# Optimization experiments

Measured on AMD Instinct MI355X. Metric: run time of the kernel, lower is better.

Reference implementation:

```python
import jax, jax.numpy as jnp
import numpy as np

SPIRAL_LEN = 12
V_LEVELS = [32768, 8192, 2048, 512, 128]
CHANNELS = [3, 32, 64, 128, 256]


def spiral_conv(x, spiral, W, b):
    # x: [B, V, C_in]; spiral: [V, S] neighbor indices
    B, V, C = x.shape
    g = x[:, spiral, :]                      # [B, V, S, C_in] irregular gather
    g = g.reshape(B, V, -1)                  # [B, V, S*C_in]
    return g @ W + b                         # [B, V, C_out]


def mesh_pool(x, idx, w):
    # sparse down_transform (<=3 nnz per row): out[b,i,:] = sum_k w[i,k] * x[b, idx[i,k], :]
    return jnp.einsum('bvkc,vk->bvc', x[:, idx, :], w)


def setup_inputs() -> dict:
    key = jax.random.key(0)
    ks = jax.random.split(key, 32)
    S = SPIRAL_LEN
    V = V_LEVELS
    C = CHANNELS
    d = {}
    d['x'] = jax.random.normal(ks[0], (32, V[0], C[0]), dtype=jnp.float32)
    for i in range(4):
        d[f'spiral{i}'] = jax.random.randint(ks[1 + i], (V[i], S), 0, V[i])
        d[f'didx{i}'] = jax.random.randint(ks[5 + i], (V[i + 1], 3), 0, V[i])
        w = jax.random.uniform(ks[9 + i], (V[i + 1], 3), dtype=jnp.float32)
        d[f'dw{i}'] = w / w.sum(-1, keepdims=True)  # barycentric-like rows
        fan_in = S * C[i]
        d[f'W{i}'] = jax.random.normal(ks[13 + i], (fan_in, C[i + 1]), dtype=jnp.float32) * np.float32(1.0 / np.sqrt(fan_in))
        d[f'b{i}'] = jnp.zeros((C[i + 1],), jnp.float32)
    flat_in = V[4] * C[4]  # num_vert * out_channels[-2]
    d['Wl1'] = jax.random.normal(ks[20], (flat_in, 512), dtype=jnp.float32) * np.float32(1.0 / np.sqrt(flat_in))
    d['bl1'] = jnp.zeros((512,), jnp.float32)
    d['Wl2'] = jax.random.normal(ks[21], (512, 64), dtype=jnp.float32) * np.float32(1.0 / np.sqrt(512))
    d['bl2'] = jnp.zeros((64,), jnp.float32)
    return d


def reference(x, spiral0, spiral1, spiral2, spiral3,
              didx0, didx1, didx2, didx3,
              dw0, dw1, dw2, dw3,
              W0, b0, W1, b1, W2, b2, W3, b3,
              Wl1, bl1, Wl2, bl2):
    spirals = (spiral0, spiral1, spiral2, spiral3)
    didx = (didx0, didx1, didx2, didx3)
    dw = (dw0, dw1, dw2, dw3)
    Wb = ((W0, b0), (W1, b1), (W2, b2), (W3, b3))
    for i in range(4):  # SpiralEnblock: elu(spiral_conv(x)) -> sparse pool
        x = jax.nn.elu(spiral_conv(x, spirals[i], *Wb[i]))
        x = mesh_pool(x, didx[i], dw[i])
    B = x.shape[0]
    x = x.reshape(B, -1)                     # [B, num_vert * C_last]
    x = jax.nn.elu(x @ Wl1 + bl1)            # [B, 512]
    y = x @ Wl2 + bl2                        # [B, latent]
    return (x, y)
```

## Files before the change

kernel.cpp:

```cpp
#include <hip/hip_runtime.h>
#include <cstdint>
#include <cstddef>

typedef _Float16 f16x8 __attribute__((ext_vector_type(8)));
typedef _Float16 f16x4 __attribute__((ext_vector_type(4)));
typedef float f32x4 __attribute__((ext_vector_type(4)));

static __device__ __forceinline__ float elu_f(float t) {
    return t > 0.0f ? t : expm1f(t);
}

static __device__ __forceinline__ int block_pu0(int bid, int P, int vshift_out, int nbl)
{
    if (nbl < 0) return bid * P;
    int xcd  = bid & 7;
    int slot = bid >> 3;
    int nb   = slot & ((1 << nbl) - 1);
    int tile = slot >> nbl;
    return ((xcd + (nb << 3)) << vshift_out) + tile * P;
}

template<int KTOT, int C_OUT, int BN>
__global__ __launch_bounds__(256)
void prep_w(const float* __restrict__ W, _Float16* __restrict__ o)
{
    constexpr int KT = KTOT/64;
    int i = blockIdx.x * 256 + threadIdx.x;
    if (i >= KTOT*C_OUT) return;
    int j = i & 7;
    int rest = i >> 3;
    int n = rest % BN;
    int kc = (rest / BN) & 7;
    int t = (rest / (BN*8)) % KT;
    int y = rest / (BN*8*KT);
    int k = t*64 + kc*8 + j;
    o[i] = (_Float16)W[(size_t)k*C_OUT + y*BN + n];
}

__global__ __launch_bounds__(256)
void prep_w0(const float* __restrict__ W, _Float16* __restrict__ o)
{
    int i = blockIdx.x * 256 + threadIdx.x;
    if (i >= 2048) return;
    int j = i & 7;
    int n = (i >> 3) & 31;
    int kc = i >> 8;
    int k = kc*8 + j;
    int s = k >> 2, c = k & 3;
    float v = (s < 12 && c < 3) ? W[(size_t)(s*3 + c)*32 + n] : 0.0f;
    o[i] = (_Float16)v;
}

__global__ __launch_bounds__(256)
void prep_xT(const float* __restrict__ x, _Float16* __restrict__ xT)
{
    __shared__ _Float16 t[16][64*4 + 8];
    const int v0 = blockIdx.x * 64;
    const int tid = threadIdx.x;
    #pragma unroll
    for (int it = 0; it < 4; ++it) {
        int e = it*256 + tid;
        int b = e >> 6, v = e & 63;
        const float* p = x + ((size_t)b*32768 + v0 + v)*3;
        f16x4 h;
        h[0] = (_Float16)p[0]; h[1] = (_Float16)p[1];
        h[2] = (_Float16)p[2]; h[3] = (_Float16)0.f;
        *(f16x4*)&t[b][v*4] = h;
    }
    __syncthreads();
    #pragma unroll
    for (int it = 0; it < 2; ++it) {
        int e = it*256 + tid;
        int vl = e >> 3, s = e & 7;
        f16x4 a = *(const f16x4*)&t[2*s][vl*4];
        f16x4 b = *(const f16x4*)&t[2*s+1][vl*4];
        f16x8 h;
        h[0]=a[0]; h[1]=a[1]; h[2]=a[2]; h[3]=a[3];
        h[4]=b[0]; h[5]=b[1]; h[6]=b[2]; h[7]=b[3];
        *(f16x8*)&xT[((size_t)(v0+vl)*16 + s*2)*4] = h;
    }
}

__global__ __launch_bounds__(256)
void prep_gidx(const int* __restrict__ didx, const int* __restrict__ spiral,
               unsigned int* __restrict__ g)
{
    int i = blockIdx.x*256 + threadIdx.x;
    if (i >= 24576*8) return;
    int q = i & 7;
    int row = i >> 3;
    unsigned int val = 0;
    if (q < 6) {
        int v = didx[row];
        unsigned int s0 = (unsigned int)spiral[v*12 + q*2];
        unsigned int s1 = (unsigned int)spiral[v*12 + q*2 + 1];
        val = s0 | (s1 << 16);
    }
    g[i] = val;
}

__global__ __launch_bounds__(256)
void conv0T(const _Float16* __restrict__ xT, const unsigned int* __restrict__ gidx,
            const _Float16* __restrict__ Wp, const float* __restrict__ bias,
            const float* __restrict__ dwt, _Float16* __restrict__ out)
{
    __shared__ _Float16 Ep[4][512];
    const int tid  = threadIdx.x;
    const int wave = tid >> 6;
    const int lane = tid & 63;
    const int quad = lane >> 4;
    const int l16  = lane & 15;
    const int u0   = blockIdx.x * 8 + wave * 2;

    f16x8 bf[2][2];
    #pragma unroll
    for (int kt = 0; kt < 2; ++kt)
        #pragma unroll
        for (int nt = 0; nt < 2; ++nt)
            bf[kt][nt] = *(const f16x8*)&Wp[(((kt*4+quad)*32) + nt*16 + l16)*8];
    float bv[2] = { bias[l16], bias[16 + l16] };

    #pragma unroll
    for (int ui = 0; ui < 2; ++ui) {
        int u = u0 + ui;
        f32x4 pacc[2] = {{0.f,0.f,0.f,0.f},{0.f,0.f,0.f,0.f}};
        #pragma unroll
        for (int kp = 0; kp < 3; ++kp) {
            int r = u*3 + kp;
            unsigned int gp0 = gidx[r*8 + quad];
            unsigned int gp1 = gidx[r*8 + 4 + quad];
            f16x4 a0 = *(const f16x4*)&xT[(size_t)(gp0 & 0xffffu)*64 + l16*4];
            f16x4 a1 = *(const f16x4*)&xT[(size_t)(gp0 >> 16)*64 + l16*4];
            f16x4 a2 = *(const f16x4*)&xT[(size_t)(gp1 & 0xffffu)*64 + l16*4];
            f16x4 a3 = *(const f16x4*)&xT[(size_t)(gp1 >> 16)*64 + l16*4];
            f16x8 af0, af1;
            af0[0]=a0[0]; af0[1]=a0[1]; af0[2]=a0[2]; af0[3]=a0[3];
            af0[4]=a1[0]; af0[5]=a1[1]; af0[6]=a1[2]; af0[7]=a1[3];
            af1[0]=a2[0]; af1[1]=a2[1]; af1[2]=a2[2]; af1[3]=a2[3];
            af1[4]=a3[0]; af1[5]=a3[1]; af1[6]=a3[2]; af1[7]=a3[3];
            float dw = dwt[r];
            #pragma unroll
            for (int nt = 0; nt < 2; ++nt) {
                f32x4 m = {0.f,0.f,0.f,0.f};
                m = __builtin_amdgcn_mfma_f32_16x16x32_f16(af0, bf[0][nt], m, 0,0,0);
                m = __builtin_amdgcn_mfma_f32_16x16x32_f16(af1, bf[1][nt], m, 0,0,0);
                #pragma unroll
                for (int rr = 0; rr < 4; ++rr)
                    pacc[nt][rr] += dw * elu_f(m[rr] + bv[nt]);
            }
        }
        #pragma unroll
        for (int nt = 0; nt < 2; ++nt)
            #pragma unroll
            for (int rr = 0; rr < 4; ++rr)
                Ep[wave][(quad*4+rr)*32 + nt*16 + l16] = (_Float16)pacc[nt][rr];
        int b  = lane >> 2;
        int c8 = lane & 3;
        f16x8 rowv = *(const f16x8*)&Ep[wave][b*32 + c8*8];
        *(f16x8*)&out[(size_t)b*262144 + (size_t)u*32 + c8*8] = rowv;
    }
}

template<int C_IN, int C_OUT, int P, int BN, int WGM, int WGN, bool OUT_HALF>
__global__ __launch_bounds__(256)
void conv_pool_mfma(const _Float16* __restrict__ x, const int* __restrict__ spiral,
                    const _Float16* __restrict__ Wp, const float* __restrict__ bias,
                    const int* __restrict__ didx, const float* __restrict__ dwt,
                    void* __restrict__ outv, int vshift_in, int vshift_out, int nbl)
{
    constexpr int R    = 3*P;
    constexpr int KTOT = 12*C_IN;
    constexpr int KT   = KTOT/64;
    constexpr int NST  = KT*2;
    constexpr int WTM  = R/WGM;
    constexpr int WTN  = BN/WGN;
    constexpr int NMT  = WTM/16;
    constexpr int NNT  = WTN/16;
    constexpr int C4   = BN/4;
    static_assert(WTM % 16 == 0 && WTN % 16 == 0, "tile");
    static_assert(R <= 256 && (P*C4) % 256 == 0, "loops");

    __shared__ unsigned short gidx[R*12];
    __shared__ _Float16 E[R*(BN+4)];

    const int tid  = threadIdx.x;
    const int wave = tid >> 6;
    const int lane = tid & 63;
    const int quad = lane >> 4;
    const int l16  = lane & 15;
    const int wm   = wave / WGN;
    const int wn   = wave % WGN;
    const int pu0  = block_pu0(blockIdx.x, P, vshift_out, nbl);
    const int n0   = blockIdx.y * BN;
    const int vmask_out = (1 << vshift_out) - 1;
    const int base_in = (pu0 >> vshift_out) << vshift_in;

    if (tid < R) {
        int ul = tid / 3;
        int kp = tid - ul*3;
        int u  = (pu0 + ul) & vmask_out;
        int v  = didx[u*3 + kp];
        const int* svp = spiral + v*12;
        #pragma unroll
        for (int j = 0; j < 12; ++j) gidx[tid*12 + j] = (unsigned short)svp[j];
    }
    __syncthreads();

    f32x4 acc[NMT][NNT];
    #pragma unroll
    for (int i = 0; i < NMT; ++i)
        #pragma unroll
        for (int j = 0; j < NNT; ++j) acc[i][j] = (f32x4){0.f, 0.f, 0.f, 0.f};

    const _Float16* xb = x + (size_t)base_in * C_IN;

    auto loadStep = [&](int s, f16x8* af, f16x8* bf) {
        const int k0 = s*32;
        const int sv = k0 / C_IN;
        const int c  = (k0 & (C_IN-1)) + quad*8;
        #pragma unroll
        for (int i = 0; i < NMT; ++i) {
            int m_local = wm*WTM + i*16 + l16;
            int g = gidx[m_local*12 + sv];
            af[i] = *(const f16x8*)&xb[(size_t)g*C_IN + c];
        }
        const _Float16* wsrc = Wp + ((size_t)(blockIdx.y*NST + s)*4 + quad)*BN*8;
        #pragma unroll
        for (int j = 0; j < NNT; ++j) {
            int n_local = wn*WTN + j*16 + l16;
            bf[j] = *(const f16x8*)&wsrc[n_local*8];
        }
    };
    auto mfmaStep = [&](const f16x8* af, const f16x8* bf) {
        #pragma unroll
        for (int i = 0; i < NMT; ++i)
            #pragma unroll
            for (int j = 0; j < NNT; ++j)
                acc[i][j] = __builtin_amdgcn_mfma_f32_16x16x32_f16(
                    af[i], bf[j], acc[i][j], 0, 0, 0);
    };

    f16x8 afA[NMT], bfA[NNT], afB[NMT], bfB[NNT];
    loadStep(0, afA, bfA);
    for (int st = 0; st < NST; st += 2) {
        loadStep(st + 1, afB, bfB);
        mfmaStep(afA, bfA);
        if (st + 2 < NST) loadStep(st + 2, afA, bfA);
        mfmaStep(afB, bfB);
    }

    float bv[NNT];
    #pragma unroll
    for (int j = 0; j < NNT; ++j)
        bv[j] = bias[n0 + wn*WTN + j*16 + l16];

    #pragma unroll
    for (int i = 0; i < NMT; ++i) {
        int row_base = wm*WTM + i*16 + quad*4;
        #pragma unroll
        for (int j = 0; j < NNT; ++j) {
            int col = wn*WTN + j*16 + l16;
            #pragma unroll
            for (int r = 0; r < 4; ++r)
                E[(size_t)(row_base + r)*(BN+4) + col] =
                    (_Float16)elu_f(acc[i][j][r] + bv[j]);
        }
    }
    __syncthreads();

    #pragma unroll
    for (int e = tid; e < P*C4; e += 256) {
        int ul = e / C4;
        int c4 = e - ul*C4;
        int pu = pu0 + ul;
        int u  = pu & vmask_out;
        const float* w = dwt + u*3;
        f16x4 a0 = *(const f16x4*)&E[(size_t)(ul*3 + 0)*(BN+4) + c4*4];
        f16x4 a1 = *(const f16x4*)&E[(size_t)(ul*3 + 1)*(BN+4) + c4*4];
        f16x4 a2 = *(const f16x4*)&E[(size_t)(ul*3 + 2)*(BN+4) + c4*4];
        float ox = w[0]*(float)a0[0] + w[1]*(float)a1[0] + w[2]*(float)a2[0];
        float oy = w[0]*(float)a0[1] + w[1]*(float)a1[1] + w[2]*(float)a2[1];
        float oz = w[0]*(float)a0[2] + w[1]*(float)a1[2] + w[2]*(float)a2[2];
        float ow = w[0]*(float)a0[3] + w[1]*(float)a1[3] + w[2]*(float)a2[3];
        if (OUT_HALF) {
            f16x4 h; h[0]=(_Float16)ox; h[1]=(_Float16)oy; h[2]=(_Float16)oz; h[3]=(_Float16)ow;
            *(f16x4*)&((_Float16*)outv)[(size_t)pu*C_OUT + n0 + c4*4] = h;
        } else {
            float4 o; o.x=ox; o.y=oy; o.z=oz; o.w=ow;
            *(float4*)&((float*)outv)[(size_t)pu*C_OUT + n0 + c4*4] = o;
        }
    }
}

__global__ __launch_bounds__(256)
void fc1_partial(const float* __restrict__ xflat, const float* __restrict__ Wl1,
                 float* __restrict__ partial)
{
    __shared__ float sb[8704];
    const int tid = threadIdx.x;
    const int n4 = tid & 31;
    const int kq = (tid >> 5) & 3;
    const int mh = tid >> 7;
    const int nt = blockIdx.x;
    const int ks = blockIdx.y;
    const int kbase = ks * 128;

    for (int e = tid; e < 1024; e += 256) {
        int m = e >> 5, k4 = e & 31;
        *(float4*)&sb[m*128 + k4*4] = *(const float4*)&xflat[(size_t)m*32768 + kbase + k4*4];
    }
    __syncthreads();

    float acc[16][4];
    #pragma unroll
    for (int m = 0; m < 16; ++m)
        #pragma unroll
        for (int c = 0; c < 4; ++c) acc[m][c] = 0.0f;

    const float* Wb = Wl1 + (size_t)(kbase + kq*32)*512 + nt*128 + n4*4;
    #pragma unroll 2
    for (int i = 0; i < 32; i += 4) {
        float4 w0 = *(const float4*)(Wb + (size_t)(i+0)*512);
        float4 w1 = *(const float4*)(Wb + (size_t)(i+1)*512);
        float4 w2 = *(const float4*)(Wb + (size_t)(i+2)*512);
        float4 w3 = *(const float4*)(Wb + (size_t)(i+3)*512);
        #pragma unroll
        for (int m = 0; m < 16; ++m) {
            float4 xv = *(const float4*)&sb[(mh*16 + m)*128 + kq*32 + i];
            acc[m][0] += xv.x*w0.x + xv.y*w1.x + xv.z*w2.x + xv.w*w3.x;
            acc[m][1] += xv.x*w0.y + xv.y*w1.y + xv.z*w2.y + xv.w*w3.y;
            acc[m][2] += xv.x*w0.z + xv.y*w1.z + xv.z*w2.z + xv.w*w3.z;
            acc[m][3] += xv.x*w0.w + xv.y*w1.w + xv.z*w2.w + xv.w*w3.w;
        }
    }
    __syncthreads();

    int slot = (mh*2 + (kq >> 1))*32 + n4;
    if (kq & 1) {
        #pragma unroll
        for (int m = 0; m < 16; ++m)
            *(float4*)&sb[slot*68 + m*4] = *(float4*)&acc[m][0];
    }
    __syncthreads();
    if (!(kq & 1)) {
        #pragma unroll
        for (int m = 0; m < 16; ++m) {
            float4 v = *(const float4*)&sb[slot*68 + m*4];
            acc[m][0] += v.x; acc[m][1] += v.y; acc[m][2] += v.z; acc[m][3] += v.w;
        }
    }
    __syncthreads();
    int slot2 = mh*32 + n4;
    if (kq == 2) {
        #pragma unroll
        for (int m = 0; m < 16; ++m)
            *(float4*)&sb[slot2*68 + m*4] = *(float4*)&acc[m][0];
    }
    __syncthreads();
    if (kq == 0) {
        float* pb = partial + ((size_t)(ks*4 + nt)*32 + mh*16)*128 + n4*4;
        #pragma unroll
        for (int m = 0; m < 16; ++m) {
            float4 v = *(const float4*)&sb[slot2*68 + m*4];
            float4 o;
            o.x = acc[m][0] + v.x; o.y = acc[m][1] + v.y;
            o.z = acc[m][2] + v.z; o.w = acc[m][3] + v.w;
            *(float4*)(pb + (size_t)m*128) = o;
        }
    }
}

__global__ __launch_bounds__(256)
void fc1_reduce(const float* __restrict__ partial, const float* __restrict__ bl1,
                float* __restrict__ hout)
{
    int i = blockIdx.x * 256 + threadIdx.x;
    int m = i >> 9, n = i & 511;
    int nt = n >> 7, nl = n & 127;
    const float* p = partial + ((size_t)nt*32 + m)*128 + nl;
    float s = 0.0f;
    #pragma unroll 8
    for (int ks = 0; ks < 256; ++ks)
        s += p[(size_t)ks*4*4096];
    hout[i] = elu_f(s + bl1[n]);
}

__global__ __launch_bounds__(64)
void fc2_kernel(const float* __restrict__ h, const float* __restrict__ Wl2,
                const float* __restrict__ bl2, float* __restrict__ y)
{
    int m = blockIdx.x;
    int n = threadIdx.x;
    float s = bl2[n];
    for (int k = 0; k < 512; ++k)
        s += h[(size_t)m*512 + k] * Wl2[(size_t)k*64 + n];
    y[(size_t)m*64 + n] = s;
}

extern "C" void kernel_launch(void* const* d_in, const int* in_sizes, int n_in,
                              void* d_out, int out_size, void* d_ws, size_t ws_size,
                              hipStream_t stream)
{
    (void)in_sizes; (void)n_in; (void)out_size; (void)ws_size;

    const float* x0 = (const float*)d_in[0];
    const int*   sp[4]; const int* didx[4]; const float* dwp[4];
    const float* Wp[4]; const float* bp[4];
    for (int i = 0; i < 4; ++i) {
        sp[i]   = (const int*)  d_in[1 + i*5 + 0];
        didx[i] = (const int*)  d_in[1 + i*5 + 1];
        dwp[i]  = (const float*)d_in[1 + i*5 + 2];
        Wp[i]   = (const float*)d_in[1 + i*5 + 3];
        bp[i]   = (const float*)d_in[1 + i*5 + 4];
    }
    const float* Wl1 = (const float*)d_in[21];
    const float* bl1 = (const float*)d_in[22];
    const float* Wl2 = (const float*)d_in[23];
    const float* bl2 = (const float*)d_in[24];
    float* out = (float*)d_out;

    char* wsb = (char*)d_ws;
    float* persist      = (float*)wsb;
    float* partial      = (float*)(wsb + (4<<20));
    _Float16* xT        = (_Float16*)(wsb + (24<<20));
    _Float16* pooled0   = (_Float16*)(wsb + (32<<20));
    _Float16* pooled1   = (_Float16*)(wsb + (48<<20));
    _Float16* pooled2   = (_Float16*)(wsb + (56<<20));
    unsigned int* gidx0 = (unsigned int*)(wsb + (60<<20));
    _Float16* w0h       = (_Float16*)(wsb + (61<<20));
    _Float16* w1h       = w0h + 2048;
    _Float16* w2h       = w1h + 24576;
    _Float16* w3h       = w2h + 98304;

    prep_w0<<<8, 256, 0, stream>>>(Wp[0], w0h);
    prep_w< 384,  64,  64><<<( 24576 + 255)/256, 256, 0, stream>>>(Wp[1], w1h);
    prep_w< 768, 128, 128><<<( 98304 + 255)/256, 256, 0, stream>>>(Wp[2], w2h);
    prep_w<1536, 256,  64><<<(393216 + 255)/256, 256, 0, stream>>>(Wp[3], w3h);
    prep_gidx<<<768, 256, 0, stream>>>(didx[0], sp[0], gidx0);

    for (int h = 0; h < 2; ++h) {
        _Float16* xTh = xT + (size_t)h*2097152;
        prep_xT<<<512, 256, 0, stream>>>(x0 + (size_t)h*16*98304, xTh);
        conv0T<<<1024, 256, 0, stream>>>(xTh, gidx0, w0h, bp[0], dwp[0],
                                         pooled0 + (size_t)h*16*262144);
    }

    conv_pool_mfma<32,64,64,64,4,1,true><<<1024, 256, 0, stream>>>(
        pooled0, sp[1], w1h, bp[1], didx[1], dwp[1], pooled1, 13, 11, 2);

    conv_pool_mfma<64,128,32,128,2,2,true><<<512, 256, 0, stream>>>(
        pooled1, sp[2], w2h, bp[2], didx[2], dwp[2], pooled2, 11, 9, 2);

    conv_pool_mfma<128,256,32,64,2,2,false><<<dim3(128, 4), 256, 0, stream>>>(
        pooled2, sp[3], w3h, bp[3], didx[3], dwp[3], persist, 9, 7, 2);

    fc1_partial<<<dim3(4, 256), 256, 0, stream>>>(persist, Wl1, partial);
    fc1_reduce<<<64, 256, 0, stream>>>(partial, bl1, out);

    fc2_kernel<<<32, 64, 0, stream>>>(out, Wl2, bl2, out + 16384);
}
```

Baseline: 332.1 us.

## Deepen conv_pool register prefetch to four stages and halve block tile sizes

Adds a templated four-deep register prefetch pipeline to the MFMA spiral-conv kernel, so three K-steps of gathered A and W fragments are in flight while one is being multiplied. It also halves the pooled-vertex tile per block, reshapes the wave grid, doubles the grid size of the three conv layers, and adds a min-4-blocks occupancy hint to launch bounds. The aim is to hide gather latency and raise occupancy. In exchange it uses more registers per thread, which the occupancy hint may force into spills, and smaller tiles give less reuse of weight fragments.

```diff
diff --git a/kernel.cpp b/kernel.cpp
--- a/kernel.cpp
+++ b/kernel.cpp
@@ -161,8 +161,8 @@
     }
 }
 
-template<int C_IN, int C_OUT, int P, int BN, int WGM, int WGN, bool OUT_HALF>
-__global__ __launch_bounds__(256)
+template<int C_IN, int C_OUT, int P, int BN, int WGM, int WGN, bool OUT_HALF, int PIPE>
+__global__ __launch_bounds__(256, 4)
 void conv_pool_mfma(const _Float16* __restrict__ x, const int* __restrict__ spiral,
                     const _Float16* __restrict__ Wp, const float* __restrict__ bias,
                     const int* __restrict__ didx, const float* __restrict__ dwt,
@@ -179,6 +179,9 @@
     constexpr int C4   = BN/4;
     static_assert(WTM % 16 == 0 && WTN % 16 == 0, "tile");
     static_assert(R <= 256 && (P*C4) % 256 == 0, "loops");
+    static_assert(PIPE == 2 || PIPE == 4, "pipe");
+    static_assert(PIPE != 2 || NST % 2 == 0, "pipe2");
+    static_assert(PIPE != 4 || NST % 4 == 0, "pipe4");
 
     __shared__ unsigned short gidx[R*12];
     __shared__ _Float16 E[R*(BN+4)];
@@ -240,13 +243,31 @@
                     af[i], bf[j], acc[i][j], 0, 0, 0);
     };
 
-    f16x8 afA[NMT], bfA[NNT], afB[NMT], bfB[NNT];
-    loadStep(0, afA, bfA);
-    for (int st = 0; st < NST; st += 2) {
-        loadStep(st + 1, afB, bfB);
-        mfmaStep(afA, bfA);
-        if (st + 2 < NST) loadStep(st + 2, afA, bfA);
-        mfmaStep(afB, bfB);
+    if constexpr (PIPE == 2) {
+        f16x8 afA[NMT], bfA[NNT], afB[NMT], bfB[NNT];
+        loadStep(0, afA, bfA);
+        for (int st = 0; st < NST; st += 2) {
+            loadStep(st + 1, afB, bfB);
+            mfmaStep(afA, bfA);
+            if (st + 2 < NST) loadStep(st + 2, afA, bfA);
+            mfmaStep(afB, bfB);
+        }
+    } else {
+        f16x8 afA[NMT], bfA[NNT], afB[NMT], bfB[NNT];
+        f16x8 afC[NMT], bfC[NNT], afD[NMT], bfD[NNT];
+        loadStep(0, afA, bfA);
+        loadStep(1, afB, bfB);
+        loadStep(2, afC, bfC);
+        for (int st = 0; st < NST; st += 4) {
+            loadStep(st + 3, afD, bfD);
+            mfmaStep(afA, bfA);
+            if (st + 4 < NST) loadStep(st + 4, afA, bfA);
+            mfmaStep(afB, bfB);
+            if (st + 5 < NST) loadStep(st + 5, afB, bfB);
+            mfmaStep(afC, bfC);
+            if (st + 6 < NST) loadStep(st + 6, afC, bfC);
+            mfmaStep(afD, bfD);
+        }
     }
 
     float bv[NNT];
@@ -445,13 +466,13 @@
                                          pooled0 + (size_t)h*16*262144);
     }
 
-    conv_pool_mfma<32,64,64,64,4,1,true><<<1024, 256, 0, stream>>>(
+    conv_pool_mfma<32,64,32,64,2,2,true,4><<<2048, 256, 0, stream>>>(
         pooled0, sp[1], w1h, bp[1], didx[1], dwp[1], pooled1, 13, 11, 2);
 
-    conv_pool_mfma<64,128,32,128,2,2,true><<<512, 256, 0, stream>>>(
+    conv_pool_mfma<64,128,16,128,1,4,true,4><<<1024, 256, 0, stream>>>(
         pooled1, sp[2], w2h, bp[2], didx[2], dwp[2], pooled2, 11, 9, 2);
 
-    conv_pool_mfma<128,256,32,64,2,2,false><<<dim3(128, 4), 256, 0, stream>>>(
+    conv_pool_mfma<128,256,16,64,1,4,false,4><<<dim3(256, 4), 256, 0, stream>>>(
         pooled2, sp[3], w3h, bp[3], didx[3], dwp[3], persist, 9, 7, 2);
 
     fc1_partial<<<dim3(4, 256), 256, 0, stream>>>(persist, Wl1, partial);
```

New measurement: 384.5 us. +15.8%, slower.

## Stage spiral-gathered A and weight tiles through LDS with async global_load_lds double buffering

Applied to the files above, without the earlier changes.

Replaces the register-level direct global loads of gathered activations and packed weights with asynchronous global_load_lds copies into double-buffered, XOR-swizzled LDS tiles. Each k-group is staged one iteration ahead while MFMAs consume the current buffer, and the epilogue buffer E now aliases the staging memory. The goal is to overlap the irregular gather latency with compute and cut per-lane global traffic. In exchange it adds a block barrier per group and raises LDS usage, which may reduce occupancy.

```diff
diff --git a/kernel.cpp b/kernel.cpp
--- a/kernel.cpp
+++ b/kernel.cpp
@@ -8,6 +8,13 @@
 
 static __device__ __forceinline__ float elu_f(float t) {
     return t > 0.0f ? t : expm1f(t);
+}
+
+typedef __attribute__((address_space(1))) const unsigned int guint;
+typedef __attribute__((address_space(3))) unsigned int       luint;
+static __device__ __forceinline__ void gload_lds16(const void* g, void* l)
+{
+    __builtin_amdgcn_global_load_lds((guint*)g, (luint*)l, 16, 0, 0);
 }
 
 static __device__ __forceinline__ int block_pu0(int bid, int P, int vshift_out, int nbl)
@@ -177,11 +184,29 @@
     constexpr int NMT  = WTM/16;
     constexpr int NNT  = WTN/16;
     constexpr int C4   = BN/4;
+    constexpr int GS   = (C_IN == 32) ? 1 : 2;
+    constexpr int NG   = NST / GS;
+    constexpr int CPR  = GS * 4;
+    constexpr int CPRS = (CPR == 4) ? 2 : 3;
+    constexpr int ACH  = R * CPR;
+    constexpr int BCH  = GS * BN * 4;
+    constexpr int AIPW = ACH / 256;
+    constexpr int BIPW = BCH / 256;
+    constexpr int ASUBH = R * GS * 32;
+    constexpr int BSUBH = GS * 32 * BN;
     static_assert(WTM % 16 == 0 && WTN % 16 == 0, "tile");
     static_assert(R <= 256 && (P*C4) % 256 == 0, "loops");
-
-    __shared__ unsigned short gidx[R*12];
-    __shared__ _Float16 E[R*(BN+4)];
+    static_assert(ACH % 256 == 0 && BCH % 256 == 0, "stage");
+    static_assert(NST % GS == 0 && GS*32 <= C_IN, "group");
+
+    constexpr size_t BUFB = (size_t)(2*ASUBH + 2*BSUBH) * 2;
+    constexpr size_t EB   = (size_t)R * (BN + 4) * 2;
+    constexpr size_t GOFF = (BUFB > EB ? BUFB : EB);
+    __shared__ __align__(16) char smem[GOFF + (size_t)R*12*2];
+    _Float16* Ab = (_Float16*)smem;
+    _Float16* Bb = (_Float16*)(smem + (size_t)2*ASUBH*2);
+    unsigned short* gidx = (unsigned short*)(smem + GOFF);
+    _Float16* E = (_Float16*)smem;
 
     const int tid  = threadIdx.x;
     const int wave = tid >> 6;
@@ -214,39 +239,64 @@
 
     const _Float16* xb = x + (size_t)base_in * C_IN;
 
-    auto loadStep = [&](int s, f16x8* af, f16x8* bf) {
-        const int k0 = s*32;
-        const int sv = k0 / C_IN;
-        const int c  = (k0 & (C_IN-1)) + quad*8;
-        #pragma unroll
-        for (int i = 0; i < NMT; ++i) {
-            int m_local = wm*WTM + i*16 + l16;
-            int g = gidx[m_local*12 + sv];
-            af[i] = *(const f16x8*)&xb[(size_t)g*C_IN + c];
-        }
-        const _Float16* wsrc = Wp + ((size_t)(blockIdx.y*NST + s)*4 + quad)*BN*8;
-        #pragma unroll
-        for (int j = 0; j < NNT; ++j) {
-            int n_local = wn*WTN + j*16 + l16;
-            bf[j] = *(const f16x8*)&wsrc[n_local*8];
-        }
+    auto SWZ = [](int r) -> int {
+        return (CPR == 4) ? ((r & 3) ^ ((r >> 2) & 3)) : (r & 7);
     };
-    auto mfmaStep = [&](const f16x8* af, const f16x8* bf) {
-        #pragma unroll
-        for (int i = 0; i < NMT; ++i)
+
+    auto stage = [&](int g, int buf) {
+        const int k0g = g * GS * 32;
+        const int sv  = k0g / C_IN;
+        const int c0  = k0g % C_IN;
+        _Float16* Ad = Ab + (size_t)buf * ASUBH;
+        #pragma unroll
+        for (int i = 0; i < AIPW; ++i) {
+            int t  = (wave*AIPW + i)*64 + lane;
+            int r  = t >> CPRS;
+            int q  = t & (CPR - 1);
+            int qq = q ^ SWZ(r);
+            int gr = gidx[r*12 + sv];
+            gload_lds16(xb + (size_t)gr*C_IN + c0 + qq*8,
+                        Ad + (size_t)(wave*AIPW + i)*512);
+        }
+        _Float16* Bd = Bb + (size_t)buf * BSUBH;
+        const _Float16* bs = Wp + ((size_t)(blockIdx.y*NST + g*GS)*4)*BN*8;
+        #pragma unroll
+        for (int i = 0; i < BIPW; ++i) {
+            int t = (wave*BIPW + i)*64 + lane;
+            gload_lds16(bs + (size_t)t*8,
+                        Bd + (size_t)(wave*BIPW + i)*512);
+        }
+    };
+
+    stage(0, 0);
+    __syncthreads();
+
+    for (int g = 0; g < NG; ++g) {
+        const int cur = g & 1;
+        if (g + 1 < NG) stage(g + 1, cur ^ 1);
+        const _Float16* Ar = Ab + (size_t)cur * ASUBH;
+        const _Float16* Br = Bb + (size_t)cur * BSUBH;
+        #pragma unroll
+        for (int sl = 0; sl < GS; ++sl) {
+            f16x8 af[NMT], bf[NNT];
             #pragma unroll
-            for (int j = 0; j < NNT; ++j)
-                acc[i][j] = __builtin_amdgcn_mfma_f32_16x16x32_f16(
-                    af[i], bf[j], acc[i][j], 0, 0, 0);
-    };
-
-    f16x8 afA[NMT], bfA[NNT], afB[NMT], bfB[NNT];
-    loadStep(0, afA, bfA);
-    for (int st = 0; st < NST; st += 2) {
-        loadStep(st + 1, afB, bfB);
-        mfmaStep(afA, bfA);
-        if (st + 2 < NST) loadStep(st + 2, afA, bfA);
-        mfmaStep(afB, bfB);
+            for (int i = 0; i < NMT; ++i) {
+                int m = wm*WTM + i*16 + l16;
+                af[i] = *(const f16x8*)&Ar[(size_t)(m*CPR + ((sl*4 + quad) ^ SWZ(m)))*8];
+            }
+            #pragma unroll
+            for (int j = 0; j < NNT; ++j) {
+                int n = wn*WTN + j*16 + l16;
+                bf[j] = *(const f16x8*)&Br[(size_t)((sl*4 + quad)*BN + n)*8];
+            }
+            #pragma unroll
+            for (int i = 0; i < NMT; ++i)
+                #pragma unroll
+                for (int j = 0; j < NNT; ++j)
+                    acc[i][j] = __builtin_amdgcn_mfma_f32_16x16x32_f16(
+                        af[i], bf[j], acc[i][j], 0, 0, 0);
+        }
+        __syncthreads();
     }
 
     float bv[NNT];
```

Result: faster. 292.9 us (-11.8%).
